# Kernel tuning notes

Hardware: AMD Instinct MI355X
Metric: run time of the kernel (lower is better)

## Reference

```python
import jax, jax.numpy as jnp
import numpy as np

EPS = 1e-5

def prelu(x, a):
    return jnp.where(x >= 0, x, a * x)

def batch_norm(x, axes):
    # training-mode BatchNorm with gamma=1, beta=0 (init values)
    m = jnp.mean(x, axis=axes, keepdims=True)
    v = jnp.var(x, axis=axes, keepdims=True)
    return (x - m) / jnp.sqrt(v + EPS)

def conv_branch(X, w, b):
    # X: [B,N,F]; Conv2d(1,1,(1,k)) over the feature axis, VALID
    lhs = X[:, None, :, :]                      # [B,1,N,F]
    rhs = w.reshape(1, 1, 1, -1)                # OIHW
    out = jax.lax.conv_general_dilated(lhs, rhs, (1, 1), 'VALID',
        dimension_numbers=('NCHW', 'OIHW', 'NCHW'))
    return out[:, 0] + b                        # [B,N,F-k+1]

def setup_inputs() -> dict:
    key = jax.random.key(0)
    ks = jax.random.split(key, 16)
    B, N, F, H, D = 8192, 29, 147, 4, 128
    d_cat = 429
    s = 0.05
    return {
        'X': jax.random.normal(ks[0], (B, N, F), jnp.float32),
        'corr': jax.random.uniform(ks[1], (B, N, N), jnp.float32),
        'w_c1': s * jax.random.normal(ks[2], (3,), jnp.float32),
        'b_c1': jnp.zeros((1,), jnp.float32),
        'w_c2': s * jax.random.normal(ks[3], (5,), jnp.float32),
        'b_c2': jnp.zeros((1,), jnp.float32),
        'w_c3': s * jax.random.normal(ks[4], (7,), jnp.float32),
        'b_c3': jnp.zeros((1,), jnp.float32),
        'a_cnn': 0.25 * jnp.ones((1,), jnp.float32),
        'Wg': s * jax.random.normal(ks[5], (d_cat, D), jnp.float32),
        'bg': jnp.zeros((D,), jnp.float32),
        'a_gnn': 0.25 * jnp.ones((1,), jnp.float32),
        'centroids': jax.random.normal(ks[6], (H, 1, D), jnp.float32),
        'head_w': s * jax.random.normal(ks[7], (H,), jnp.float32),
        'Wp': s * jax.random.normal(ks[8], (D, D), jnp.float32),
        'bp': jnp.zeros((D,), jnp.float32),
        'Wm1': s * jax.random.normal(ks[9], (D, D), jnp.float32),
        'bm1': jnp.zeros((D,), jnp.float32),
        'a_mlp': 0.25 * jnp.ones((1,), jnp.float32),
        'Wm2': s * jax.random.normal(ks[10], (D, 1), jnp.float32),
        'bm2': jnp.zeros((1,), jnp.float32),
    }

def reference(X, corr, w_c1, b_c1, w_c2, b_c2, w_c3, b_c3, a_cnn,
              Wg, bg, a_gnn, centroids, head_w, Wp, bp,
              Wm1, bm1, a_mlp, Wm2, bm2):
    # three conv branches + concat + PReLU + BN over node channels
    a1 = conv_branch(X, w_c1, b_c1)             # [B,29,145]
    a2 = conv_branch(X, w_c2, b_c2)             # [B,29,143]
    a3 = conv_branch(X, w_c3, b_c3)             # [B,29,141]
    x = prelu(jnp.concatenate([a1, a2, a3], axis=2), a_cnn)  # [B,29,429]
    x = batch_norm(x, (0, 2))
    # GraphConv: A x W + b
    x = jnp.einsum('bnm,bmd->bnd', corr, x) @ Wg + bg        # [B,29,128]
    x = prelu(x, a_gnn)
    x = batch_norm(x, (0, 2))
    # CoSimPool: multi-head cosine-sim attention assignment to 1 cluster
    xn = x / (jnp.linalg.norm(x, axis=-1, keepdims=True) + 1e-8)
    cn = centroids / (jnp.linalg.norm(centroids, axis=-1, keepdims=True) + 1e-8)
    sim = jnp.einsum('hmd,bnd->bhmn', cn, xn)                # [B,4,1,29]
    agg = jnp.einsum('h,bhmn->bmn', head_w, sim)             # 1x1 conv over heads
    C = jax.nn.softmax(agg, axis=-1)                         # [B,1,29]
    x = jnp.einsum('bmn,bnd->bmd', C, x) @ Wp + bp           # [B,1,128]
    x = x[:, 0]                                              # squeeze(1)
    x = batch_norm(x, (0,))
    h = prelu(x @ Wm1 + bm1, a_mlp)
    y = jax.nn.sigmoid(h @ Wm2 + bm2)                        # [B,1]
    return y
```

## Files before the change

kernel.cpp:

```cpp
#include <hip/hip_runtime.h>

#define B_    8192
#define N_    29
#define F_    147
#define DC    429
#define D_    128
#define ROWS  (B_*N_)
#define EPSBN 1e-5f

#define UTSTR   4096
#define RS_SH   3712

#define X3_OFF   16777216
#define ACC_OFF  (X3_OFF + B_*D_)
#define BN1_OFF  (ACC_OFF)
#define BN2_OFF  (ACC_OFF + 1856)
#define BN3_OFF  (ACC_OFF + 3712)
#define FIN_OFF  (ACC_OFF + 11904)
#define M1_OFF   (FIN_OFF + 0)
#define IS1_OFF  (FIN_OFF + 32)
#define M2_OFF   (FIN_OFF + 64)
#define IS2_OFF  (FIN_OFF + 96)
#define M3_OFF   (FIN_OFF + 128)
#define IS3_OFF  (FIN_OFF + 256)
#define CSW_OFF  (FIN_OFF + 384)
#define V_OFF    (FIN_OFF + 512)
#define V1_OFF   (FIN_OFF + 640)
#define IMG_OFF  (FIN_OFF + 1024)

typedef __bf16 bf16x8 __attribute__((ext_vector_type(8)));
typedef float  f32x4  __attribute__((ext_vector_type(4)));

__device__ __forceinline__ unsigned short f2bf(float f) {
  unsigned int u = __float_as_uint(f);
  u += 0x7fffu + ((u >> 16) & 1u);
  return (unsigned short)(u >> 16);
}
__device__ __forceinline__ float bf2f(unsigned u16) {
  return __uint_as_float(u16 << 16);
}

#define TSTR 456
#define UTILS 34

__global__ void k0a_img(const float* __restrict__ Wg, float* __restrict__ ws)
{
  __shared__ float cs_l[8];
  const int tid = threadIdx.x;
  const int kb = blockIdx.x * 8;
  if (tid < 8) cs_l[tid] = 0.f;
  __syncthreads();
  unsigned short* img = (unsigned short*)(ws + IMG_OFF);
  for (int i = tid; i < 8*448; i += 256) {
    int kk = i / 448, dk = i - kk*448;
    int k = kb + kk;
    int d;
    if      (dk < 145)  d = dk;
    else if (dk == 145) d = -1;
    else if (dk < 289)  d = dk - 1;
    else if (dk == 289) d = -1;
    else if (dk < 431)  d = dk - 2;
    else                d = -1;
    float v = (d >= 0) ? Wg[(size_t)d*D_ + k] : 0.f;
    img[(size_t)k*448 + dk] = f2bf(v);
    if (d >= 0) atomicAdd(&cs_l[kk], v);
  }
  __syncthreads();
  if (tid < 8) ws[CSW_OFF + kb + tid] = cs_l[tid];
}

__global__ void k0b_cent(const float* __restrict__ cent, const float* __restrict__ hw,
                         float* __restrict__ ws)
{
  __shared__ float sq[128];
  __shared__ float nrm;
  const int tid = threadIdx.x;
  float vk = 0.f;
  for (int h = 0; h < 4; ++h) {
    float c = cent[h*D_ + tid];
    sq[tid] = c*c;
    __syncthreads();
    if (tid == 0) { float s=0.f; for (int j=0;j<128;++j) s+=sq[j]; nrm = sqrtf(s)+1e-8f; }
    __syncthreads();
    vk += hw[h] * c / nrm;
    __syncthreads();
  }
  ws[V_OFF + tid] = vk;
  sq[tid] = vk;
  __syncthreads();
  if (tid == 0) { float s=0.f; for (int j=0;j<128;++j) s+=sq[j]; ws[V1_OFF] = s; }
}

__global__ __launch_bounds__(512, 2) void k1_conv_gemm(
    const float* __restrict__ X,
    const float* __restrict__ wc1, const float* __restrict__ bc1,
    const float* __restrict__ wc2, const float* __restrict__ bc2,
    const float* __restrict__ wc3, const float* __restrict__ bc3,
    const float* __restrict__ acnn, float* __restrict__ ws)
{
  __shared__ __align__(16) unsigned short t_s[64*TSTR];
  const int tid = threadIdx.x;
  const int b0 = blockIdx.x * 2;

  for (int i = tid; i < 2*3*448; i += 512) {
    int bb = i / (3*448), rem = i - bb*(3*448);
    int r = rem / 448, c = rem - r*448;
    t_s[(bb*32 + 29 + r)*TSTR + c] = 0;
  }
  for (int i = tid; i < 58*19; i += 512) {
    int rr = i / 19, j = i - rr*19;
    int bb = (rr >= 29), n = rr - bb*29;
    int col = (j == 0) ? 145 : ((j == 1) ? 289 : (429 + j));
    t_s[(bb*32 + n)*TSTR + col] = 0;
  }

  const float c10 = wc1[0], c11 = wc1[1], c12 = wc1[2], b1 = bc1[0];
  const float c20 = wc2[0], c21 = wc2[1], c22 = wc2[2], c23 = wc2[3], c24 = wc2[4], b2 = bc2[0];
  const float c30 = wc3[0], c31 = wc3[1], c32 = wc3[2], c33 = wc3[3], c34 = wc3[4],
              c35 = wc3[5], c36 = wc3[6], b3 = bc3[0];
  const float ap = acnn[0];

  {
    const int r = tid >> 3, q = tid & 7;
    const int bb = r >> 5, n = r & 31;
    const int f0 = q * 19;
    float s1 = 0.f, s2 = 0.f;
    const bool act = (n < 29);
    if (act) {
      const int cnt = min(19, 145 - f0);
      const int n2 = min(cnt, 143 - f0);
      const int n3 = min(cnt, 141 - f0);
      const float* xr = X + (size_t)((b0 + bb)*N_ + n) * F_;
      unsigned short* tr = t_s + (bb*32 + n)*TSTR;
      float wA=xr[f0],wB=xr[f0+1],wC=xr[f0+2],wD=xr[f0+3],wE=xr[f0+4],wF=xr[f0+5],wG;
      #pragma unroll
      for (int i2 = 0; i2 < 19; ++i2) {
        if (i2 < cnt) {
          int f = f0 + i2;
          wG = (f + 6 < F_) ? xr[f+6] : 0.f;
          float v1 = fmaf(wA,c10, fmaf(wB,c11, fmaf(wC,c12, b1)));
          v1 = (v1 >= 0.f) ? v1 : ap*v1;
          s1 += v1; s2 = fmaf(v1, v1, s2);
          tr[f] = f2bf(v1);
          if (i2 < n2) {
            float v2 = fmaf(wA,c20, fmaf(wB,c21, fmaf(wC,c22, fmaf(wD,c23, fmaf(wE,c24, b2)))));
            v2 = (v2 >= 0.f) ? v2 : ap*v2;
            s1 += v2; s2 = fmaf(v2, v2, s2);
            tr[146+f] = f2bf(v2);
          }
          if (i2 < n3) {
            float v3 = fmaf(wA,c30, fmaf(wB,c31, fmaf(wC,c32, fmaf(wD,c33, fmaf(wE,c34, fmaf(wF,c35, fmaf(wG,c36, b3)))))));
            v3 = (v3 >= 0.f) ? v3 : ap*v3;
            s1 += v3; s2 = fmaf(v3, v3, s2);
            tr[290+f] = f2bf(v3);
          }
          wA=wB; wB=wC; wC=wD; wD=wE; wE=wF; wF=wG;
        }
      }
    }
    #pragma unroll
    for (int off = 4; off >= 1; off >>= 1) {
      s1 += __shfl_xor(s1, off);
      s2 += __shfl_xor(s2, off);
    }
    if (act && q == 0) {
      float* bn1 = ws + BN1_OFF + (size_t)(blockIdx.x & 31) * 58;
      atomicAdd(&bn1[n*2+0], s1);
      atomicAdd(&bn1[n*2+1], s2);
    }
  }
  __syncthreads();

  const int wv = tid >> 6, lane = tid & 63;
  const int lrow = lane & 15, quad = lane >> 4;
  const int bb = wv >> 2;
  const int n0 = (wv & 3) * 32;
  const unsigned short* imgp = (const unsigned short*)(ws + IMG_OFF);
  const unsigned short* gB0 = imgp + (size_t)(n0 + lrow)*448 + quad*8;
  const unsigned short* gB1 = gB0 + 16*448;
  const unsigned short* tA = t_s + (size_t)(bb*32)*TSTR + quad*8;

  f32x4 a00 = (f32x4){0.f,0.f,0.f,0.f}, a01 = a00, a10 = a00, a11 = a00;
  bf16x8 Bc0 = *(const bf16x8*)(gB0);
  bf16x8 Bc1 = *(const bf16x8*)(gB1);
  #pragma unroll
  for (int ks = 0; ks < 14; ++ks) {
    bf16x8 Bn0, Bn1;
    if (ks < 13) {
      Bn0 = *(const bf16x8*)(gB0 + (ks+1)*32);
      Bn1 = *(const bf16x8*)(gB1 + (ks+1)*32);
    }
    bf16x8 A0 = *(const bf16x8*)(tA + lrow*TSTR + ks*32);
    bf16x8 A1 = *(const bf16x8*)(tA + (16+lrow)*TSTR + ks*32);
    a00 = __builtin_amdgcn_mfma_f32_16x16x32_bf16(A0, Bc0, a00, 0, 0, 0);
    a01 = __builtin_amdgcn_mfma_f32_16x16x32_bf16(A0, Bc1, a01, 0, 0, 0);
    a10 = __builtin_amdgcn_mfma_f32_16x16x32_bf16(A1, Bc0, a10, 0, 0, 0);
    a11 = __builtin_amdgcn_mfma_f32_16x16x32_bf16(A1, Bc1, a11, 0, 0, 0);
    Bc0 = Bn0; Bc1 = Bn1;
  }
  __syncthreads();

  {
    unsigned short* ut = t_s + bb*4352;
    const int fb0 = n0 + lrow, fb1 = n0 + 16 + lrow;
    #pragma unroll
    for (int i = 0; i < 4; ++i) {
      int m0 = quad*4 + i, m1 = 16 + quad*4 + i;
      ut[fb0*UTILS + m0] = f2bf(a00[i]);
      ut[fb1*UTILS + m0] = f2bf(a01[i]);
      ut[fb0*UTILS + m1] = f2bf(a10[i]);
      ut[fb1*UTILS + m1] = f2bf(a11[i]);
    }
  }
  __syncthreads();
  {
    const unsigned* u32t = (const unsigned*)t_s;
    unsigned short* ws16 = (unsigned short*)ws;
    #pragma unroll
    for (int it = 0; it < 8; ++it) {
      int idx = tid + it*512;
      int bbs = idx >> 11, rem = idx & 2047;
      int f = rem >> 4, pr = rem & 15;
      unsigned* Ug = (unsigned*)(ws16 + (size_t)(b0 + bbs)*UTSTR);
      Ug[f*16 + pr] = u32t[bbs*2176 + f*17 + pr];
    }
  }
}

__global__ void k2_bn1(float* __restrict__ ws) {
  const int k = threadIdx.x;
  if (k < 29) {
    float s1 = 0.f, s2 = 0.f;
    for (int s = 0; s < 32; ++s) {
      s1 += ws[BN1_OFF + s*58 + k*2 + 0];
      s2 += ws[BN1_OFF + s*58 + k*2 + 1];
    }
    const float inv = 1.f / (float)(B_ * DC);
    float mean = s1 * inv;
    float var  = s2 * inv - mean * mean;
    ws[M1_OFF  + k] = mean;
    ws[IS1_OFF + k] = rsqrtf(var + EPSBN);
  }
}

__global__ __launch_bounds__(256) void k3_gnn(
    const float* __restrict__ corr, const float* __restrict__ bg,
    const float* __restrict__ agnn, float* __restrict__ ws)
{
  __shared__ float cwf[841];
  __shared__ unsigned short a_s[32*40];
  __shared__ float m1s[29], is1s[29], cms[29], st1s[29], st2s[29], svs[29];

  const int b = blockIdx.x, tid = threadIdx.x;
  const int wv = tid >> 6, lane = tid & 63;
  const int lrow = lane & 15, quad = lane >> 4;
  unsigned short* Utb = (unsigned short*)ws + (size_t)b * UTSTR;

  if (tid < 29) {
    m1s[tid] = ws[M1_OFF+tid]; is1s[tid] = ws[IS1_OFF+tid];
    st1s[tid] = 0.f; st2s[tid] = 0.f; svs[tid] = 0.f;
  }
  const float* cb = corr + (size_t)b * 841;
  for (int i = tid; i < 841; i += 256) cwf[i] = cb[i];
  __syncthreads();

  const int f0 = wv * 32;
  bf16x8 B0 = *(const bf16x8*)&Utb[(f0      + lrow)*32 + quad*8];
  bf16x8 B1 = *(const bf16x8*)&Utb[(f0 + 16 + lrow)*32 + quad*8];

  for (int i = tid; i < 1024; i += 256) {
    int n = i >> 5, m = i & 31;
    float v = (n < 29 && m < 29) ? cwf[n*29 + m] * is1s[m] : 0.f;
    a_s[n*40 + m] = f2bf(v);
  }
  if (tid < 29) {
    float cm = 0.f;
    for (int m = 0; m < 29; ++m) cm = fmaf(cwf[tid*29 + m] * is1s[m], m1s[m], cm);
    cms[tid] = cm;
  }
  __syncthreads();

  bf16x8 A0 = *(const bf16x8*)&a_s[lrow*40 + quad*8];
  bf16x8 A1 = *(const bf16x8*)&a_s[(16 + lrow)*40 + quad*8];
  f32x4 acc[2][2];
  acc[0][0] = (f32x4){0.f,0.f,0.f,0.f}; acc[0][1] = (f32x4){0.f,0.f,0.f,0.f};
  acc[1][0] = (f32x4){0.f,0.f,0.f,0.f}; acc[1][1] = (f32x4){0.f,0.f,0.f,0.f};
  acc[0][0] = __builtin_amdgcn_mfma_f32_16x16x32_bf16(A0, B0, acc[0][0], 0, 0, 0);
  acc[0][1] = __builtin_amdgcn_mfma_f32_16x16x32_bf16(A0, B1, acc[0][1], 0, 0, 0);
  acc[1][0] = __builtin_amdgcn_mfma_f32_16x16x32_bf16(A1, B0, acc[1][0], 0, 0, 0);
  acc[1][1] = __builtin_amdgcn_mfma_f32_16x16x32_bf16(A1, B1, acc[1][1], 0, 0, 0);
  __syncthreads();

  const float ag = agnn[0];
  const float vA  = ws[V_OFF  + f0 + lrow],      vB  = ws[V_OFF  + f0 + 16 + lrow];
  const float csA = ws[CSW_OFF + f0 + lrow],     csB = ws[CSW_OFF + f0 + 16 + lrow];
  const float bgA = bg[f0 + lrow],               bgB = bg[f0 + 16 + lrow];
  #pragma unroll
  for (int mt = 0; mt < 2; ++mt) {
    #pragma unroll
    for (int i = 0; i < 4; ++i) {
      int n = mt*16 + quad*4 + i;
      if (n < 29) {
        float y0 = acc[mt][0][i] - cms[n]*csA + bgA;
        float y1 = acc[mt][1][i] - cms[n]*csB + bgB;
        y0 = (y0 >= 0.f) ? y0 : ag*y0;
        y1 = (y1 >= 0.f) ? y1 : ag*y1;
        Utb[n*D_ + f0 + lrow]      = f2bf(y0);
        Utb[n*D_ + f0 + 16 + lrow] = f2bf(y1);
        float sy  = y0 + y1;
        float sy2 = fmaf(y0, y0, y1*y1);
        float sv  = fmaf(y0, vA, y1*vB);
        #pragma unroll
        for (int off = 8; off >= 1; off >>= 1) {
          sy  += __shfl_xor(sy, off);
          sy2 += __shfl_xor(sy2, off);
          sv  += __shfl_xor(sv, off);
        }
        if (lrow == 0) {
          atomicAdd(&st1s[n], sy);
          atomicAdd(&st2s[n], sy2);
          atomicAdd(&svs[n],  sv);
        }
      }
    }
  }
  __syncthreads();
  if (tid < 29) {
    float* rs = (float*)(Utb + RS_SH);
    rs[tid]      = st1s[tid];
    rs[29 + tid] = st2s[tid];
    rs[58 + tid] = svs[tid];
    float* bn2 = ws + BN2_OFF + (size_t)(b & 31) * 58;
    atomicAdd(&bn2[tid*2+0], st1s[tid]);
    atomicAdd(&bn2[tid*2+1], st2s[tid]);
  }
}

__global__ void k3_finalize2(float* __restrict__ ws) {
  const int n = threadIdx.x;
  if (n < 29) {
    float s1 = 0.f, s2 = 0.f;
    for (int s = 0; s < 32; ++s) {
      s1 += ws[BN2_OFF + s*58 + n*2 + 0];
      s2 += ws[BN2_OFF + s*58 + n*2 + 1];
    }
    const float inv = 1.f / (float)(B_ * D_);
    float mean = s1 * inv, var = s2 * inv - mean * mean;
    ws[M2_OFF + n] = mean;
    ws[IS2_OFF + n] = rsqrtf(var + EPSBN);
  }
}

__global__ __launch_bounds__(256) void k4_pool(
    const float* __restrict__ Wp, const float* __restrict__ bpv,
    float* __restrict__ ws)
{
  __shared__ float cs_s[4*32];
  __shared__ float pool_s[4*128];
  const int tid = threadIdx.x, wv = tid >> 6, lane = tid & 63;
  const int b = blockIdx.x * 4 + wv;
  const unsigned short* yb = (const unsigned short*)ws + (size_t)b * UTSTR;
  const float* rs = (const float*)(yb + RS_SH);
  const float V1 = ws[V1_OFF];

  float agg = -1e30f, m2 = 0.f, is2 = 0.f;
  if (lane < 29) {
    float S1 = rs[lane], S2 = rs[29+lane], Sv = rs[58+lane];
    m2 = ws[M2_OFF + lane]; is2 = ws[IS2_OFF + lane];
    float ss = fmaxf(S2 - 2.f*m2*S1 + 128.f*m2*m2, 0.f);
    float rn = sqrtf(ss);
    agg = (is2*(Sv - m2*V1)) / (is2*rn + 1e-8f);
  }
  float mx = agg;
  #pragma unroll
  for (int off = 32; off >= 1; off >>= 1) mx = fmaxf(mx, __shfl_xor(mx, off));
  float e = (lane < 29) ? __expf(agg - mx) : 0.f;
  float den = e, kof = e*is2*m2;
  #pragma unroll
  for (int off = 32; off >= 1; off >>= 1) { den += __shfl_xor(den, off); kof += __shfl_xor(kof, off); }
  float rden = 1.f / den;
  float koff = kof * rden;
  if (lane < 32) cs_s[wv*32 + lane] = (lane < 29) ? e*is2*rden : 0.f;
  __syncthreads();

  const unsigned* y32 = (const unsigned*)yb;
  float p0 = -koff, p1 = -koff;
  #pragma unroll
  for (int n = 0; n < 29; ++n) {
    float c = cs_s[wv*32 + n];
    unsigned u = y32[n*64 + lane];
    p0 = fmaf(c, bf2f(u & 0xffffu), p0);
    p1 = fmaf(c, bf2f(u >> 16), p1);
  }
  pool_s[wv*128 + 2*lane]     = p0;
  pool_s[wv*128 + 2*lane + 1] = p1;
  __syncthreads();

  float a0 = bpv[lane], a1 = bpv[64 + lane];
  const float* ps = pool_s + wv*128;
  #pragma unroll 4
  for (int j = 0; j < 128; ++j) {
    float p = ps[j];
    a0 = fmaf(p, Wp[j*D_ + lane], a0);
    a1 = fmaf(p, Wp[j*D_ + 64 + lane], a1);
  }
  ws[X3_OFF + (size_t)b*D_ + lane]      = a0;
  ws[X3_OFF + (size_t)b*D_ + 64 + lane] = a1;
  float* bn3 = ws + BN3_OFF + (size_t)(b & 31) * 256;
  atomicAdd(&bn3[lane*2+0], a0);
  atomicAdd(&bn3[lane*2+1], a0*a0);
  atomicAdd(&bn3[(64+lane)*2+0], a1);
  atomicAdd(&bn3[(64+lane)*2+1], a1*a1);
}

__global__ void k4_finalize3(float* __restrict__ ws) {
  const int k = threadIdx.x;
  float s1 = 0.f, s2 = 0.f;
  for (int s = 0; s < 32; ++s) {
    s1 += ws[BN3_OFF + s*256 + k*2 + 0];
    s2 += ws[BN3_OFF + s*256 + k*2 + 1];
  }
  const float inv = 1.f / (float)B_;
  float mean = s1 * inv, var = s2 * inv - mean * mean;
  ws[M3_OFF + k] = mean;
  ws[IS3_OFF + k] = rsqrtf(var + EPSBN);
}

__global__ __launch_bounds__(128) void k5_mlp(
    const float* __restrict__ Wm1, const float* __restrict__ bm1,
    const float* __restrict__ amlp, const float* __restrict__ Wm2,
    const float* __restrict__ bm2, const float* __restrict__ ws,
    float* __restrict__ out)
{
  __shared__ float x_s[4*128];
  __shared__ float red[4][2];
  const int b0 = blockIdx.x * 4, k = threadIdx.x;
  const float m3 = ws[M3_OFF + k], is3 = ws[IS3_OFF + k];
  #pragma unroll
  for (int bb = 0; bb < 4; ++bb)
    x_s[bb*128 + k] = (ws[X3_OFF + (size_t)(b0+bb)*D_ + k] - m3) * is3;
  __syncthreads();
  float h0 = bm1[k], h1 = h0, h2 = h0, h3 = h0;
  #pragma unroll 4
  for (int j = 0; j < 128; ++j) {
    float w = Wm1[j*D_ + k];
    h0 = fmaf(x_s[j],       w, h0);
    h1 = fmaf(x_s[128 + j], w, h1);
    h2 = fmaf(x_s[256 + j], w, h2);
    h3 = fmaf(x_s[384 + j], w, h3);
  }
  const float am = amlp[0];
  const float w2 = Wm2[k];
  h0 = ((h0 >= 0.f) ? h0 : am*h0) * w2;
  h1 = ((h1 >= 0.f) ? h1 : am*h1) * w2;
  h2 = ((h2 >= 0.f) ? h2 : am*h2) * w2;
  h3 = ((h3 >= 0.f) ? h3 : am*h3) * w2;
  #pragma unroll
  for (int off = 32; off >= 1; off >>= 1) {
    h0 += __shfl_down(h0, off);
    h1 += __shfl_down(h1, off);
    h2 += __shfl_down(h2, off);
    h3 += __shfl_down(h3, off);
  }
  if ((k & 63) == 0) {
    int w = k >> 6;
    red[0][w] = h0; red[1][w] = h1; red[2][w] = h2; red[3][w] = h3;
  }
  __syncthreads();
  if (k < 4) {
    float logit = red[k][0] + red[k][1] + bm2[0];
    out[b0 + k] = 1.f / (1.f + expf(-logit));
  }
}

extern "C" void kernel_launch(void* const* d_in, const int* in_sizes, int n_in,
                              void* d_out, int out_size, void* d_ws, size_t ws_size,
                              hipStream_t stream)
{
  (void)in_sizes; (void)n_in; (void)out_size; (void)ws_size;
  const float* X    = (const float*)d_in[0];
  const float* corr = (const float*)d_in[1];
  const float* wc1  = (const float*)d_in[2];
  const float* bc1  = (const float*)d_in[3];
  const float* wc2  = (const float*)d_in[4];
  const float* bc2  = (const float*)d_in[5];
  const float* wc3  = (const float*)d_in[6];
  const float* bc3  = (const float*)d_in[7];
  const float* acnn = (const float*)d_in[8];
  const float* Wg   = (const float*)d_in[9];
  const float* bg   = (const float*)d_in[10];
  const float* agnn = (const float*)d_in[11];
  const float* cent = (const float*)d_in[12];
  const float* hw   = (const float*)d_in[13];
  const float* Wp   = (const float*)d_in[14];
  const float* bp   = (const float*)d_in[15];
  const float* Wm1  = (const float*)d_in[16];
  const float* bm1  = (const float*)d_in[17];
  const float* amlp = (const float*)d_in[18];
  const float* Wm2  = (const float*)d_in[19];
  const float* bm2  = (const float*)d_in[20];
  float* ws  = (float*)d_ws;
  float* out = (float*)d_out;

  hipMemsetAsync(ws + ACC_OFF, 0, 11904 * sizeof(float), stream);
  k0a_img<<<16, 256, 0, stream>>>(Wg, ws);
  k0b_cent<<<1, 128, 0, stream>>>(cent, hw, ws);
  k1_conv_gemm<<<B_/2, 512, 0, stream>>>(X, wc1, bc1, wc2, bc2, wc3, bc3, acnn, ws);
  k2_bn1<<<1, 32, 0, stream>>>(ws);
  k3_gnn<<<B_, 256, 0, stream>>>(corr, bg, agnn, ws);
  k3_finalize2<<<1, 32, 0, stream>>>(ws);
  k4_pool<<<B_/4, 256, 0, stream>>>(Wp, bp, ws);
  k4_finalize3<<<1, 128, 0, stream>>>(ws);
  k5_mlp<<<B_/4, 128, 0, stream>>>(Wm1, bm1, amlp, Wm2, bm2, ws, out);
}
```

Baseline: 492.7 us.

## Fold BN finalize kernels into consumers and use bf16 MFMA for pool and MLP GEMMs

Removes the three single-block BN finalize kernels by having each consumer kernel reduce the partial sums itself. The pool and MLP stages now handle 32 batches per block and do the Wp and Wm1 projections with bf16 MFMA, using transposed bf16 weight images prepared in the setup kernel. The pooled-mean offset is folded in through a column-sum correction. The conv stage now preloads each thread's X window into registers, with a separate tail path for the last chunk. The cost is lower precision in the pool and MLP GEMMs and redundant per-block finalize reductions.

New measurement: 479.5 us. 1.03x faster.

```diff
diff --git a/kernel.cpp b/kernel.cpp
--- a/kernel.cpp
+++ b/kernel.cpp
@@ -17,16 +17,13 @@
 #define BN2_OFF  (ACC_OFF + 1856)
 #define BN3_OFF  (ACC_OFF + 3712)
 #define FIN_OFF  (ACC_OFF + 11904)
-#define M1_OFF   (FIN_OFF + 0)
-#define IS1_OFF  (FIN_OFF + 32)
-#define M2_OFF   (FIN_OFF + 64)
-#define IS2_OFF  (FIN_OFF + 96)
-#define M3_OFF   (FIN_OFF + 128)
-#define IS3_OFF  (FIN_OFF + 256)
 #define CSW_OFF  (FIN_OFF + 384)
 #define V_OFF    (FIN_OFF + 512)
 #define V1_OFF   (FIN_OFF + 640)
+#define CSWP_OFF (FIN_OFF + 768)
 #define IMG_OFF  (FIN_OFF + 1024)
+#define WPI_OFF  (IMG_OFF + 28672)
+#define WM1I_OFF (WPI_OFF + 8192)
 
 typedef __bf16 bf16x8 __attribute__((ext_vector_type(8)));
 typedef float  f32x4  __attribute__((ext_vector_type(4)));
@@ -42,31 +39,52 @@
 
 #define TSTR 456
 #define UTILS 34
-
-__global__ void k0a_img(const float* __restrict__ Wg, float* __restrict__ ws)
-{
-  __shared__ float cs_l[8];
+#define ATSTR 136
+
+__global__ void k0a_img(const float* __restrict__ Wg, const float* __restrict__ Wp,
+                        const float* __restrict__ Wm1, float* __restrict__ ws)
+{
   const int tid = threadIdx.x;
-  const int kb = blockIdx.x * 8;
-  if (tid < 8) cs_l[tid] = 0.f;
-  __syncthreads();
-  unsigned short* img = (unsigned short*)(ws + IMG_OFF);
-  for (int i = tid; i < 8*448; i += 256) {
-    int kk = i / 448, dk = i - kk*448;
-    int k = kb + kk;
-    int d;
-    if      (dk < 145)  d = dk;
-    else if (dk == 145) d = -1;
-    else if (dk < 289)  d = dk - 1;
-    else if (dk == 289) d = -1;
-    else if (dk < 431)  d = dk - 2;
-    else                d = -1;
-    float v = (d >= 0) ? Wg[(size_t)d*D_ + k] : 0.f;
-    img[(size_t)k*448 + dk] = f2bf(v);
-    if (d >= 0) atomicAdd(&cs_l[kk], v);
-  }
-  __syncthreads();
-  if (tid < 8) ws[CSW_OFF + kb + tid] = cs_l[tid];
+  if (blockIdx.x < 16) {
+    __shared__ float cs_l[8];
+    const int kb = blockIdx.x * 8;
+    if (tid < 8) cs_l[tid] = 0.f;
+    __syncthreads();
+    unsigned short* img = (unsigned short*)(ws + IMG_OFF);
+    for (int i = tid; i < 8*448; i += 256) {
+      int kk = i / 448, dk = i - kk*448;
+      int k = kb + kk;
+      int d;
+      if      (dk < 145)  d = dk;
+      else if (dk == 145) d = -1;
+      else if (dk < 289)  d = dk - 1;
+      else if (dk == 289) d = -1;
+      else if (dk < 431)  d = dk - 2;
+      else                d = -1;
+      float v = (d >= 0) ? Wg[(size_t)d*D_ + k] : 0.f;
+      img[(size_t)k*448 + dk] = f2bf(v);
+      if (d >= 0) atomicAdd(&cs_l[kk], v);
+    }
+    __syncthreads();
+    if (tid < 8) ws[CSW_OFF + kb + tid] = cs_l[tid];
+  } else if (blockIdx.x == 16) {
+    unsigned short* wpi = (unsigned short*)(ws + WPI_OFF);
+    for (int i = tid; i < 16384; i += 256) {
+      int k = i >> 7, c = i & 127;
+      wpi[c*128 + k] = f2bf(Wp[k*128 + c]);
+    }
+    if (tid < 128) {
+      float s = 0.f;
+      for (int k = 0; k < 128; ++k) s += Wp[k*128 + tid];
+      ws[CSWP_OFF + tid] = s;
+    }
+  } else {
+    unsigned short* wmi = (unsigned short*)(ws + WM1I_OFF);
+    for (int i = tid; i < 16384; i += 256) {
+      int k = i >> 7, c = i & 127;
+      wmi[c*128 + k] = f2bf(Wm1[k*128 + c]);
+    }
+  }
 }
 
 __global__ void k0b_cent(const float* __restrict__ cent, const float* __restrict__ hw,
@@ -103,15 +121,15 @@
   const int b0 = blockIdx.x * 2;
 
   for (int i = tid; i < 2*3*448; i += 512) {
-    int bb = i / (3*448), rem = i - bb*(3*448);
+    int bbz = i / (3*448), rem = i - bbz*(3*448);
     int r = rem / 448, c = rem - r*448;
-    t_s[(bb*32 + 29 + r)*TSTR + c] = 0;
+    t_s[(bbz*32 + 29 + r)*TSTR + c] = 0;
   }
   for (int i = tid; i < 58*19; i += 512) {
     int rr = i / 19, j = i - rr*19;
-    int bb = (rr >= 29), n = rr - bb*29;
+    int bbz = (rr >= 29), n = rr - bbz*29;
     int col = (j == 0) ? 145 : ((j == 1) ? 289 : (429 + j));
-    t_s[(bb*32 + n)*TSTR + col] = 0;
+    t_s[(bbz*32 + n)*TSTR + col] = 0;
   }
 
   const float c10 = wc1[0], c11 = wc1[1], c12 = wc1[2], b1 = bc1[0];
@@ -123,38 +141,54 @@
   {
     const int r = tid >> 3, q = tid & 7;
     const int bb = r >> 5, n = r & 31;
+    const bool act = (n < 29);
     const int f0 = q * 19;
+    const int nld = act ? n : 28;
+    const float* xr = X + (size_t)((b0 + bb)*N_ + nld) * F_;
+    float xv[25];
+    #pragma unroll
+    for (int i = 0; i < 25; ++i) xv[i] = xr[min(f0 + i, 146)];
+
     float s1 = 0.f, s2 = 0.f;
-    const bool act = (n < 29);
+    unsigned short* tr = t_s + (bb*32 + n)*TSTR;
     if (act) {
-      const int cnt = min(19, 145 - f0);
-      const int n2 = min(cnt, 143 - f0);
-      const int n3 = min(cnt, 141 - f0);
-      const float* xr = X + (size_t)((b0 + bb)*N_ + n) * F_;
-      unsigned short* tr = t_s + (bb*32 + n)*TSTR;
-      float wA=xr[f0],wB=xr[f0+1],wC=xr[f0+2],wD=xr[f0+3],wE=xr[f0+4],wF=xr[f0+5],wG;
-      #pragma unroll
-      for (int i2 = 0; i2 < 19; ++i2) {
-        if (i2 < cnt) {
-          int f = f0 + i2;
-          wG = (f + 6 < F_) ? xr[f+6] : 0.f;
-          float v1 = fmaf(wA,c10, fmaf(wB,c11, fmaf(wC,c12, b1)));
+      if (q < 7) {
+        #pragma unroll
+        for (int i = 0; i < 19; ++i) {
+          float v1 = fmaf(xv[i],c10, fmaf(xv[i+1],c11, fmaf(xv[i+2],c12, b1)));
           v1 = (v1 >= 0.f) ? v1 : ap*v1;
           s1 += v1; s2 = fmaf(v1, v1, s2);
-          tr[f] = f2bf(v1);
-          if (i2 < n2) {
-            float v2 = fmaf(wA,c20, fmaf(wB,c21, fmaf(wC,c22, fmaf(wD,c23, fmaf(wE,c24, b2)))));
-            v2 = (v2 >= 0.f) ? v2 : ap*v2;
-            s1 += v2; s2 = fmaf(v2, v2, s2);
-            tr[146+f] = f2bf(v2);
-          }
-          if (i2 < n3) {
-            float v3 = fmaf(wA,c30, fmaf(wB,c31, fmaf(wC,c32, fmaf(wD,c33, fmaf(wE,c34, fmaf(wF,c35, fmaf(wG,c36, b3)))))));
-            v3 = (v3 >= 0.f) ? v3 : ap*v3;
-            s1 += v3; s2 = fmaf(v3, v3, s2);
-            tr[290+f] = f2bf(v3);
-          }
-          wA=wB; wB=wC; wC=wD; wD=wE; wE=wF; wF=wG;
+          tr[f0 + i] = f2bf(v1);
+          float v2 = fmaf(xv[i],c20, fmaf(xv[i+1],c21, fmaf(xv[i+2],c22, fmaf(xv[i+3],c23, fmaf(xv[i+4],c24, b2)))));
+          v2 = (v2 >= 0.f) ? v2 : ap*v2;
+          s1 += v2; s2 = fmaf(v2, v2, s2);
+          tr[146 + f0 + i] = f2bf(v2);
+          float v3 = fmaf(xv[i],c30, fmaf(xv[i+1],c31, fmaf(xv[i+2],c32, fmaf(xv[i+3],c33, fmaf(xv[i+4],c34, fmaf(xv[i+5],c35, fmaf(xv[i+6],c36, b3)))))));
+          v3 = (v3 >= 0.f) ? v3 : ap*v3;
+          s1 += v3; s2 = fmaf(v3, v3, s2);
+          tr[290 + f0 + i] = f2bf(v3);
+        }
+      } else {
+        #pragma unroll
+        for (int i = 0; i < 12; ++i) {
+          float v1 = fmaf(xv[i],c10, fmaf(xv[i+1],c11, fmaf(xv[i+2],c12, b1)));
+          v1 = (v1 >= 0.f) ? v1 : ap*v1;
+          s1 += v1; s2 = fmaf(v1, v1, s2);
+          tr[133 + i] = f2bf(v1);
+        }
+        #pragma unroll
+        for (int i = 0; i < 10; ++i) {
+          float v2 = fmaf(xv[i],c20, fmaf(xv[i+1],c21, fmaf(xv[i+2],c22, fmaf(xv[i+3],c23, fmaf(xv[i+4],c24, b2)))));
+          v2 = (v2 >= 0.f) ? v2 : ap*v2;
+          s1 += v2; s2 = fmaf(v2, v2, s2);
+          tr[279 + i] = f2bf(v2);
+        }
+        #pragma unroll
+        for (int i = 0; i < 8; ++i) {
+          float v3 = fmaf(xv[i],c30, fmaf(xv[i+1],c31, fmaf(xv[i+2],c32, fmaf(xv[i+3],c33, fmaf(xv[i+4],c34, fmaf(xv[i+5],c35, fmaf(xv[i+6],c36, b3)))))));
+          v3 = (v3 >= 0.f) ? v3 : ap*v3;
+          s1 += v3; s2 = fmaf(v3, v3, s2);
+          tr[423 + i] = f2bf(v3);
         }
       }
     }
@@ -227,22 +261,6 @@
   }
 }
 
-__global__ void k2_bn1(float* __restrict__ ws) {
-  const int k = threadIdx.x;
-  if (k < 29) {
-    float s1 = 0.f, s2 = 0.f;
-    for (int s = 0; s < 32; ++s) {
-      s1 += ws[BN1_OFF + s*58 + k*2 + 0];
-      s2 += ws[BN1_OFF + s*58 + k*2 + 1];
-    }
-    const float inv = 1.f / (float)(B_ * DC);
-    float mean = s1 * inv;
-    float var  = s2 * inv - mean * mean;
-    ws[M1_OFF  + k] = mean;
-    ws[IS1_OFF + k] = rsqrtf(var + EPSBN);
-  }
-}
-
 __global__ __launch_bounds__(256) void k3_gnn(
     const float* __restrict__ corr, const float* __restrict__ bg,
     const float* __restrict__ agnn, float* __restrict__ ws)
@@ -257,7 +275,16 @@
   unsigned short* Utb = (unsigned short*)ws + (size_t)b * UTSTR;
 
   if (tid < 29) {
-    m1s[tid] = ws[M1_OFF+tid]; is1s[tid] = ws[IS1_OFF+tid];
+    float s1 = 0.f, s2 = 0.f;
+    #pragma unroll 4
+    for (int s = 0; s < 32; ++s) {
+      s1 += ws[BN1_OFF + s*58 + tid*2 + 0];
+      s2 += ws[BN1_OFF + s*58 + tid*2 + 1];
+    }
+    const float inv = 1.f / (float)(B_ * DC);
+    float mean = s1 * inv;
+    float var  = s2 * inv - mean * mean;
+    m1s[tid] = mean; is1s[tid] = rsqrtf(var + EPSBN);
     st1s[tid] = 0.f; st2s[tid] = 0.f; svs[tid] = 0.f;
   }
   const float* cb = corr + (size_t)b * 841;
@@ -336,140 +363,184 @@
   }
 }
 
-__global__ void k3_finalize2(float* __restrict__ ws) {
-  const int n = threadIdx.x;
-  if (n < 29) {
+__global__ __launch_bounds__(256) void k4_pool(
+    const float* __restrict__ bpv, float* __restrict__ ws)
+{
+  __shared__ unsigned short Atile[32*ATSTR];
+  __shared__ float m2s[29], is2s[29], koffs[32];
+  const int tid = threadIdx.x, wv = tid >> 6, lane = tid & 63;
+  const int b0 = blockIdx.x * 32;
+  const unsigned short* U16 = (const unsigned short*)ws;
+
+  if (tid < 29) {
     float s1 = 0.f, s2 = 0.f;
+    #pragma unroll 4
     for (int s = 0; s < 32; ++s) {
-      s1 += ws[BN2_OFF + s*58 + n*2 + 0];
-      s2 += ws[BN2_OFF + s*58 + n*2 + 1];
+      s1 += ws[BN2_OFF + s*58 + tid*2 + 0];
+      s2 += ws[BN2_OFF + s*58 + tid*2 + 1];
     }
     const float inv = 1.f / (float)(B_ * D_);
     float mean = s1 * inv, var = s2 * inv - mean * mean;
-    ws[M2_OFF + n] = mean;
-    ws[IS2_OFF + n] = rsqrtf(var + EPSBN);
-  }
-}
-
-__global__ __launch_bounds__(256) void k4_pool(
-    const float* __restrict__ Wp, const float* __restrict__ bpv,
-    float* __restrict__ ws)
-{
-  __shared__ float cs_s[4*32];
-  __shared__ float pool_s[4*128];
+    m2s[tid] = mean; is2s[tid] = rsqrtf(var + EPSBN);
+  }
+  __syncthreads();
+
+  const float V1 = ws[V1_OFF];
+  unsigned* At32 = (unsigned*)Atile;
+  for (int mb = 0; mb < 8; ++mb) {
+    const int m = wv*8 + mb;
+    const unsigned short* yb = U16 + (size_t)(b0 + m) * UTSTR;
+    const float* rs = (const float*)(yb + RS_SH);
+    float agg = -1e30f, m2 = 0.f, is2 = 0.f;
+    if (lane < 29) {
+      float S1 = rs[lane], S2 = rs[29+lane], Sv = rs[58+lane];
+      m2 = m2s[lane]; is2 = is2s[lane];
+      float ss = fmaxf(S2 - 2.f*m2*S1 + 128.f*m2*m2, 0.f);
+      agg = (is2*(Sv - m2*V1)) / (is2*sqrtf(ss) + 1e-8f);
+    }
+    float mx = agg;
+    #pragma unroll
+    for (int off = 32; off >= 1; off >>= 1) mx = fmaxf(mx, __shfl_xor(mx, off));
+    float e = (lane < 29) ? __expf(agg - mx) : 0.f;
+    float den = e, kof = e*is2*m2;
+    #pragma unroll
+    for (int off = 32; off >= 1; off >>= 1) { den += __shfl_xor(den, off); kof += __shfl_xor(kof, off); }
+    float rden = 1.f / den;
+    float c = e * is2 * rden;
+    if (lane == 0) koffs[m] = kof * rden;
+    const unsigned* y32 = (const unsigned*)yb;
+    float p0 = 0.f, p1 = 0.f;
+    #pragma unroll
+    for (int n = 0; n < 29; ++n) {
+      float cn = __shfl(c, n);
+      unsigned u = y32[n*64 + lane];
+      p0 = fmaf(cn, bf2f(u & 0xffffu), p0);
+      p1 = fmaf(cn, bf2f(u >> 16), p1);
+    }
+    At32[m*68 + lane] = (unsigned)f2bf(p0) | ((unsigned)f2bf(p1) << 16);
+  }
+  __syncthreads();
+
+  const int lrow = lane & 15, quad = lane >> 4;
+  const int n0 = wv * 32;
+  const unsigned short* wpi = (const unsigned short*)(ws + WPI_OFF);
+  f32x4 acc[2][2];
+  acc[0][0] = (f32x4){0.f,0.f,0.f,0.f}; acc[0][1] = acc[0][0];
+  acc[1][0] = acc[0][0]; acc[1][1] = acc[0][0];
+  #pragma unroll
+  for (int ks = 0; ks < 4; ++ks) {
+    bf16x8 A0 = *(const bf16x8*)&Atile[lrow*ATSTR + ks*32 + quad*8];
+    bf16x8 A1 = *(const bf16x8*)&Atile[(16+lrow)*ATSTR + ks*32 + quad*8];
+    bf16x8 Bq0 = *(const bf16x8*)&wpi[(size_t)(n0 + lrow)*128 + ks*32 + quad*8];
+    bf16x8 Bq1 = *(const bf16x8*)&wpi[(size_t)(n0 + 16 + lrow)*128 + ks*32 + quad*8];
+    acc[0][0] = __builtin_amdgcn_mfma_f32_16x16x32_bf16(A0, Bq0, acc[0][0], 0, 0, 0);
+    acc[0][1] = __builtin_amdgcn_mfma_f32_16x16x32_bf16(A0, Bq1, acc[0][1], 0, 0, 0);
+    acc[1][0] = __builtin_amdgcn_mfma_f32_16x16x32_bf16(A1, Bq0, acc[1][0], 0, 0, 0);
+    acc[1][1] = __builtin_amdgcn_mfma_f32_16x16x32_bf16(A1, Bq1, acc[1][1], 0, 0, 0);
+  }
+
+  float* bn3 = ws + BN3_OFF + (size_t)(blockIdx.x & 31) * 256;
+  #pragma unroll
+  for (int nt = 0; nt < 2; ++nt) {
+    int col = n0 + nt*16 + lrow;
+    float cswp = ws[CSWP_OFF + col], bp = bpv[col];
+    float s1c = 0.f, s2c = 0.f;
+    #pragma unroll
+    for (int mt = 0; mt < 2; ++mt) {
+      #pragma unroll
+      for (int i = 0; i < 4; ++i) {
+        int m = mt*16 + quad*4 + i;
+        float x3 = acc[mt][nt][i] - koffs[m]*cswp + bp;
+        ws[X3_OFF + (size_t)(b0 + m)*D_ + col] = x3;
+        s1c += x3; s2c = fmaf(x3, x3, s2c);
+      }
+    }
+    s1c += __shfl_xor(s1c, 16); s1c += __shfl_xor(s1c, 32);
+    s2c += __shfl_xor(s2c, 16); s2c += __shfl_xor(s2c, 32);
+    if (quad == 0) {
+      atomicAdd(&bn3[col*2+0], s1c);
+      atomicAdd(&bn3[col*2+1], s2c);
+    }
+  }
+}
+
+__global__ __launch_bounds__(256) void k5_mlp(
+    const float* __restrict__ bm1, const float* __restrict__ amlp,
+    const float* __restrict__ Wm2, const float* __restrict__ bm2,
+    float* __restrict__ ws, float* __restrict__ out)
+{
+  __shared__ unsigned short Atile[32*ATSTR];
+  __shared__ float m3s[128], is3s[128], logit_s[32];
   const int tid = threadIdx.x, wv = tid >> 6, lane = tid & 63;
-  const int b = blockIdx.x * 4 + wv;
-  const unsigned short* yb = (const unsigned short*)ws + (size_t)b * UTSTR;
-  const float* rs = (const float*)(yb + RS_SH);
-  const float V1 = ws[V1_OFF];
-
-  float agg = -1e30f, m2 = 0.f, is2 = 0.f;
-  if (lane < 29) {
-    float S1 = rs[lane], S2 = rs[29+lane], Sv = rs[58+lane];
-    m2 = ws[M2_OFF + lane]; is2 = ws[IS2_OFF + lane];
-    float ss = fmaxf(S2 - 2.f*m2*S1 + 128.f*m2*m2, 0.f);
-    float rn = sqrtf(ss);
-    agg = (is2*(Sv - m2*V1)) / (is2*rn + 1e-8f);
-  }
-  float mx = agg;
-  #pragma unroll
-  for (int off = 32; off >= 1; off >>= 1) mx = fmaxf(mx, __shfl_xor(mx, off));
-  float e = (lane < 29) ? __expf(agg - mx) : 0.f;
-  float den = e, kof = e*is2*m2;
-  #pragma unroll
-  for (int off = 32; off >= 1; off >>= 1) { den += __shfl_xor(den, off); kof += __shfl_xor(kof, off); }
-  float rden = 1.f / den;
-  float koff = kof * rden;
-  if (lane < 32) cs_s[wv*32 + lane] = (lane < 29) ? e*is2*rden : 0.f;
-  __syncthreads();
-
-  const unsigned* y32 = (const unsigned*)yb;
-  float p0 = -koff, p1 = -koff;
-  #pragma unroll
-  for (int n = 0; n < 29; ++n) {
-    float c = cs_s[wv*32 + n];
-    unsigned u = y32[n*64 + lane];
-    p0 = fmaf(c, bf2f(u & 0xffffu), p0);
-    p1 = fmaf(c, bf2f(u >> 16), p1);
-  }
-  pool_s[wv*128 + 2*lane]     = p0;
-  pool_s[wv*128 + 2*lane + 1] = p1;
-  __syncthreads();
-
-  float a0 = bpv[lane], a1 = bpv[64 + lane];
-  const float* ps = pool_s + wv*128;
-  #pragma unroll 4
-  for (int j = 0; j < 128; ++j) {
-    float p = ps[j];
-    a0 = fmaf(p, Wp[j*D_ + lane], a0);
-    a1 = fmaf(p, Wp[j*D_ + 64 + lane], a1);
-  }
-  ws[X3_OFF + (size_t)b*D_ + lane]      = a0;
-  ws[X3_OFF + (size_t)b*D_ + 64 + lane] = a1;
-  float* bn3 = ws + BN3_OFF + (size_t)(b & 31) * 256;
-  atomicAdd(&bn3[lane*2+0], a0);
-  atomicAdd(&bn3[lane*2+1], a0*a0);
-  atomicAdd(&bn3[(64+lane)*2+0], a1);
-  atomicAdd(&bn3[(64+lane)*2+1], a1*a1);
-}
-
-__global__ void k4_finalize3(float* __restrict__ ws) {
-  const int k = threadIdx.x;
-  float s1 = 0.f, s2 = 0.f;
-  for (int s = 0; s < 32; ++s) {
-    s1 += ws[BN3_OFF + s*256 + k*2 + 0];
-    s2 += ws[BN3_OFF + s*256 + k*2 + 1];
-  }
-  const float inv = 1.f / (float)B_;
-  float mean = s1 * inv, var = s2 * inv - mean * mean;
-  ws[M3_OFF + k] = mean;
-  ws[IS3_OFF + k] = rsqrtf(var + EPSBN);
-}
-
-__global__ __launch_bounds__(128) void k5_mlp(
-    const float* __restrict__ Wm1, const float* __restrict__ bm1,
-    const float* __restrict__ amlp, const float* __restrict__ Wm2,
-    const float* __restrict__ bm2, const float* __restrict__ ws,
-    float* __restrict__ out)
-{
-  __shared__ float x_s[4*128];
-  __shared__ float red[4][2];
-  const int b0 = blockIdx.x * 4, k = threadIdx.x;
-  const float m3 = ws[M3_OFF + k], is3 = ws[IS3_OFF + k];
-  #pragma unroll
-  for (int bb = 0; bb < 4; ++bb)
-    x_s[bb*128 + k] = (ws[X3_OFF + (size_t)(b0+bb)*D_ + k] - m3) * is3;
-  __syncthreads();
-  float h0 = bm1[k], h1 = h0, h2 = h0, h3 = h0;
-  #pragma unroll 4
-  for (int j = 0; j < 128; ++j) {
-    float w = Wm1[j*D_ + k];
-    h0 = fmaf(x_s[j],       w, h0);
-    h1 = fmaf(x_s[128 + j], w, h1);
-    h2 = fmaf(x_s[256 + j], w, h2);
-    h3 = fmaf(x_s[384 + j], w, h3);
-  }
+  const int b0 = blockIdx.x * 32;
+
+  if (tid < 128) {
+    float s1 = 0.f, s2 = 0.f;
+    #pragma unroll 4
+    for (int s = 0; s < 32; ++s) {
+      s1 += ws[BN3_OFF + s*256 + tid*2 + 0];
+      s2 += ws[BN3_OFF + s*256 + tid*2 + 1];
+    }
+    const float inv = 1.f / (float)B_;
+    float mean = s1 * inv, var = s2 * inv - mean * mean;
+    m3s[tid] = mean; is3s[tid] = rsqrtf(var + EPSBN);
+  }
+  if (tid >= 128 && tid < 160) logit_s[tid-128] = 0.f;
+  __syncthreads();
+
+  for (int it = 0; it < 16; ++it) {
+    int idx = tid + it*256;
+    int row = idx >> 7, col = idx & 127;
+    float v = (ws[X3_OFF + (size_t)(b0+row)*D_ + col] - m3s[col]) * is3s[col];
+    Atile[row*ATSTR + col] = f2bf(v);
+  }
+  __syncthreads();
+
+  const int lrow = lane & 15, quad = lane >> 4;
+  const int n0 = wv * 32;
+  const unsigned short* wmi = (const unsigned short*)(ws + WM1I_OFF);
+  f32x4 acc[2][2];
+  acc[0][0] = (f32x4){0.f,0.f,0.f,0.f}; acc[0][1] = acc[0][0];
+  acc[1][0] = acc[0][0]; acc[1][1] = acc[0][0];
+  #pragma unroll
+  for (int ks = 0; ks < 4; ++ks) {
+    bf16x8 A0 = *(const bf16x8*)&Atile[lrow*ATSTR + ks*32 + quad*8];
+    bf16x8 A1 = *(const bf16x8*)&Atile[(16+lrow)*ATSTR + ks*32 + quad*8];
+    bf16x8 Bq0 = *(const bf16x8*)&wmi[(size_t)(n0 + lrow)*128 + ks*32 + quad*8];
+    bf16x8 Bq1 = *(const bf16x8*)&wmi[(size_t)(n0 + 16 + lrow)*128 + ks*32 + quad*8];
+    acc[0][0] = __builtin_amdgcn_mfma_f32_16x16x32_bf16(A0, Bq0, acc[0][0], 0, 0, 0);
+    acc[0][1] = __builtin_amdgcn_mfma_f32_16x16x32_bf16(A0, Bq1, acc[0][1], 0, 0, 0);
+    acc[1][0] = __builtin_amdgcn_mfma_f32_16x16x32_bf16(A1, Bq0, acc[1][0], 0, 0, 0);
+    acc[1][1] = __builtin_amdgcn_mfma_f32_16x16x32_bf16(A1, Bq1, acc[1][1], 0, 0, 0);
+  }
+
   const float am = amlp[0];
-  const float w2 = Wm2[k];
-  h0 = ((h0 >= 0.f) ? h0 : am*h0) * w2;
-  h1 = ((h1 >= 0.f) ? h1 : am*h1) * w2;
-  h2 = ((h2 >= 0.f) ? h2 : am*h2) * w2;
-  h3 = ((h3 >= 0.f) ? h3 : am*h3) * w2;
-  #pragma unroll
-  for (int off = 32; off >= 1; off >>= 1) {
-    h0 += __shfl_down(h0, off);
-    h1 += __shfl_down(h1, off);
-    h2 += __shfl_down(h2, off);
-    h3 += __shfl_down(h3, off);
-  }
-  if ((k & 63) == 0) {
-    int w = k >> 6;
-    red[0][w] = h0; red[1][w] = h1; red[2][w] = h2; red[3][w] = h3;
-  }
-  __syncthreads();
-  if (k < 4) {
-    float logit = red[k][0] + red[k][1] + bm2[0];
-    out[b0 + k] = 1.f / (1.f + expf(-logit));
+  float bmc[2], wm2c[2];
+  #pragma unroll
+  for (int nt = 0; nt < 2; ++nt) {
+    int col = n0 + nt*16 + lrow;
+    bmc[nt] = bm1[col]; wm2c[nt] = Wm2[col];
+  }
+  #pragma unroll
+  for (int mt = 0; mt < 2; ++mt) {
+    #pragma unroll
+    for (int i = 0; i < 4; ++i) {
+      float pm = 0.f;
+      #pragma unroll
+      for (int nt = 0; nt < 2; ++nt) {
+        float h = acc[mt][nt][i] + bmc[nt];
+        h = (h >= 0.f) ? h : am*h;
+        pm = fmaf(h, wm2c[nt], pm);
+      }
+      #pragma unroll
+      for (int off = 8; off >= 1; off >>= 1) pm += __shfl_xor(pm, off);
+      if (lrow == 0) atomicAdd(&logit_s[mt*16 + quad*4 + i], pm);
+    }
+  }
+  __syncthreads();
+  if (tid < 32) {
+    float logit = logit_s[tid] + bm2[0];
+    out[b0 + tid] = 1.f / (1.f + expf(-logit));
   }
 }
 
@@ -503,13 +574,10 @@
   float* out = (float*)d_out;
 
   hipMemsetAsync(ws + ACC_OFF, 0, 11904 * sizeof(float), stream);
-  k0a_img<<<16, 256, 0, stream>>>(Wg, ws);
+  k0a_img<<<18, 256, 0, stream>>>(Wg, Wp, Wm1, ws);
   k0b_cent<<<1, 128, 0, stream>>>(cent, hw, ws);
   k1_conv_gemm<<<B_/2, 512, 0, stream>>>(X, wc1, bc1, wc2, bc2, wc3, bc3, acnn, ws);
-  k2_bn1<<<1, 32, 0, stream>>>(ws);
   k3_gnn<<<B_, 256, 0, stream>>>(corr, bg, agnn, ws);
-  k3_finalize2<<<1, 32, 0, stream>>>(ws);
-  k4_pool<<<B_/4, 256, 0, stream>>>(Wp, bp, ws);
-  k4_finalize3<<<1, 128, 0, stream>>>(ws);
-  k5_mlp<<<B_/4, 128, 0, stream>>>(Wm1, bm1, amlp, Wm2, bm2, ws, out);
-}
+  k4_pool<<<B_/32, 256, 0, stream>>>(bp, ws);
+  k5_mlp<<<B_/32, 256, 0, stream>>>(bm1, amlp, Wm2, bm2, ws, out);
+}
```
